# Performance work log

Measured on AMD Instinct MI355X. Metric: run time of the kernel, lower is better.

Reference implementation:

```python
import jax, jax.numpy as jnp
import numpy as np
import math

NUM_HEADS = 8
EMB = 256

def setup_inputs() -> dict:
    key = jax.random.key(0)
    ks = jax.random.split(key, 9)
    B_, N, C = 1024, 64, EMB  # 16 images * 64 windows, 8x8 window, C=256
    nW = 64
    q = jax.random.normal(ks[0], (B_, N, C), dtype=jnp.float32)
    k = jax.random.normal(ks[1], (B_, N, C), dtype=jnp.float32)
    v = jax.random.normal(ks[2], (B_, N, C), dtype=jnp.float32)
    mask = jax.random.normal(ks[3], (nW, N, N), dtype=jnp.float32)
    # MLP params (Linear: y = x @ W^T + b; we store W already transposed for x @ W)
    hid = 4 * C
    s1 = 1.0 / math.sqrt(C)
    s2 = 1.0 / math.sqrt(hid)
    w1 = jax.random.uniform(ks[4], (C, hid), minval=-s1, maxval=s1, dtype=jnp.float32)
    b1 = jax.random.uniform(ks[5], (hid,), minval=-s1, maxval=s1, dtype=jnp.float32)
    w2 = jax.random.uniform(ks[6], (hid, C), minval=-s2, maxval=s2, dtype=jnp.float32)
    b2 = jax.random.uniform(ks[7], (C,), minval=-s2, maxval=s2, dtype=jnp.float32)
    return {"q": q, "k": k, "v": v, "mask": mask, "H": 64, "W": 64,
            "w1": w1, "b1": b1, "w2": w2, "b2": b2}

def reference(q, k, v, mask, H, W, w1, b1, w2, b2):
    B_, N, C = q.shape
    h = NUM_HEADS
    d = C // h
    # separate heads: (B_, h, N, d)
    qh = q.reshape(B_, N, h, d).transpose(0, 2, 1, 3)
    kh = k.reshape(B_, N, h, d).transpose(0, 2, 1, 3)
    vh = v.reshape(B_, N, h, d).transpose(0, 2, 1, 3)
    attn = jnp.einsum('bhnd,bhmd->bhnm', qh, kh)  # raw scores
    nW = mask.shape[0]
    # additive window mask BEFORE scaling (faithful to original order)
    attn = attn.reshape(B_ // nW, nW, h, N, N) + mask[None, :, None, :, :]
    attn = attn.reshape(B_, h, N, N) / math.sqrt(d)
    attn = jax.nn.softmax(attn, axis=-1)
    out = jnp.einsum('bhnm,bhmd->bhnd', attn, vh)
    out = out.transpose(0, 2, 1, 3).reshape(B_, N, C)  # recombine heads
    # linear Mlp (dropout is identity at p=0.0); torch nn.GELU is exact erf
    hmid = jax.nn.gelu(out @ w1 + b1, approximate=False)
    out = out + (hmid @ w2 + b2)
    return out
```

## Files before the change

kernel.cpp:

```cpp
#include <hip/hip_runtime.h>
#include <hip/hip_bf16.h>
#include <cstdint>
#include <cstddef>

typedef __attribute__((ext_vector_type(8))) short bf16x8;
typedef __attribute__((ext_vector_type(4))) float f32x4;

static __device__ __forceinline__ unsigned short f2bf(float f) {
    __hip_bfloat16 h = __float2bfloat16(f);
    return *reinterpret_cast<unsigned short*>(&h);
}

static __device__ __forceinline__ f32x4 mfma_bf16(bf16x8 a, bf16x8 b, f32x4 c) {
    return __builtin_amdgcn_mfma_f32_16x16x32_bf16(a, b, c, 0, 0, 0);
}

static __device__ __forceinline__ bf16x8 pack8(float4 a, float4 b) {
    bf16x8 f;
    f[0]=(short)f2bf(a.x); f[1]=(short)f2bf(a.y); f[2]=(short)f2bf(a.z); f[3]=(short)f2bf(a.w);
    f[4]=(short)f2bf(b.x); f[5]=(short)f2bf(b.y); f[6]=(short)f2bf(b.z); f[7]=(short)f2bf(b.w);
    return f;
}

static __device__ __forceinline__ float gelu_erf(float v) {
    float s = v * 0.70710678118654752f;
    float a = fabsf(s);
    float t = __builtin_amdgcn_rcpf(1.0f + 0.3275911f * a);
    float poly = ((((1.061405429f * t - 1.453152027f) * t + 1.421413741f) * t
                   - 0.284496736f) * t + 0.254829592f) * t;
    float e = 1.0f - poly * __expf(-a * a);
    float erfv = copysignf(e, s);
    return 0.5f * v * (1.0f + erfv);
}

static __device__ __forceinline__ void load_lds16(const unsigned short* g, unsigned short* l) {
    __builtin_amdgcn_global_load_lds(
        (const __attribute__((address_space(1))) unsigned int*)g,
        (__attribute__((address_space(3))) unsigned int*)l, 16, 0, 0);
}

__global__ __launch_bounds__(256) void attn_kernel(
    const float* __restrict__ q, const float* __restrict__ k,
    const float* __restrict__ v, const float* __restrict__ mask,
    float* __restrict__ xout)
{
    __shared__ unsigned short Qs[64][40];
    __shared__ unsigned short Ks[64][40];
    __shared__ unsigned short Vt[32][72];
    __shared__ unsigned short Ps[64][72];

    const int tid  = threadIdx.x;
    const int b    = blockIdx.x >> 3;
    const int h    = blockIdx.x & 7;
    const int lane = tid & 63;
    const int l15  = lane & 15;
    const int g    = lane >> 4;
    const int w    = tid >> 6;

    {
        int row = tid >> 2;
        int seg = tid & 3;
        size_t base = ((size_t)(b * 64 + row)) * 256 + h * 32 + seg * 8;

        float4 a0 = *(const float4*)(q + base);
        float4 a1 = *(const float4*)(q + base + 4);
        unsigned short* p = &Qs[row][seg * 8];
        p[0]=f2bf(a0.x); p[1]=f2bf(a0.y); p[2]=f2bf(a0.z); p[3]=f2bf(a0.w);
        p[4]=f2bf(a1.x); p[5]=f2bf(a1.y); p[6]=f2bf(a1.z); p[7]=f2bf(a1.w);

        a0 = *(const float4*)(k + base);
        a1 = *(const float4*)(k + base + 4);
        p = &Ks[row][seg * 8];
        p[0]=f2bf(a0.x); p[1]=f2bf(a0.y); p[2]=f2bf(a0.z); p[3]=f2bf(a0.w);
        p[4]=f2bf(a1.x); p[5]=f2bf(a1.y); p[6]=f2bf(a1.z); p[7]=f2bf(a1.w);

        a0 = *(const float4*)(v + base);
        a1 = *(const float4*)(v + base + 4);
        int c = seg * 8;
        Vt[c + 0][row] = f2bf(a0.x);
        Vt[c + 1][row] = f2bf(a0.y);
        Vt[c + 2][row] = f2bf(a0.z);
        Vt[c + 3][row] = f2bf(a0.w);
        Vt[c + 4][row] = f2bf(a1.x);
        Vt[c + 5][row] = f2bf(a1.y);
        Vt[c + 6][row] = f2bf(a1.z);
        Vt[c + 7][row] = f2bf(a1.w);
    }
    __syncthreads();

    f32x4 s[4];
    {
        bf16x8 aQ = *(const bf16x8*)&Qs[w * 16 + l15][g * 8];
        #pragma unroll
        for (int ct = 0; ct < 4; ++ct) {
            bf16x8 bK = *(const bf16x8*)&Ks[ct * 16 + l15][g * 8];
            f32x4 z = {0.f, 0.f, 0.f, 0.f};
            s[ct] = mfma_bf16(aQ, bK, z);
        }
    }

    const float* mbase = mask + (size_t)(b & 63) * 4096;
    const float INV = 0.17677669529663688f;
    float rsum[4];
    #pragma unroll
    for (int r = 0; r < 4; ++r) {
        int row = w * 16 + g * 4 + r;
        float pr[4];
        #pragma unroll
        for (int ct = 0; ct < 4; ++ct)
            pr[ct] = (s[ct][r] + mbase[row * 64 + ct * 16 + l15]) * INV;
        float m = fmaxf(fmaxf(pr[0], pr[1]), fmaxf(pr[2], pr[3]));
        #pragma unroll
        for (int off = 1; off < 16; off <<= 1)
            m = fmaxf(m, __shfl_xor(m, off));
        float sum = 0.f;
        #pragma unroll
        for (int ct = 0; ct < 4; ++ct) { pr[ct] = __expf(pr[ct] - m); sum += pr[ct]; }
        #pragma unroll
        for (int off = 1; off < 16; off <<= 1)
            sum += __shfl_xor(sum, off);
        rsum[r] = sum;
        #pragma unroll
        for (int ct = 0; ct < 4; ++ct)
            Ps[row][ct * 16 + l15] = f2bf(pr[ct]);
    }

    f32x4 o[2] = {};
    #pragma unroll
    for (int ks = 0; ks < 2; ++ks) {
        bf16x8 pa = *(const bf16x8*)&Ps[w * 16 + l15][ks * 32 + g * 8];
        #pragma unroll
        for (int n = 0; n < 2; ++n) {
            bf16x8 vb = *(const bf16x8*)&Vt[n * 16 + l15][ks * 32 + g * 8];
            o[n] = mfma_bf16(pa, vb, o[n]);
        }
    }

    #pragma unroll
    for (int n = 0; n < 2; ++n) {
        #pragma unroll
        for (int r = 0; r < 4; ++r) {
            int row = w * 16 + g * 4 + r;
            xout[((size_t)(b * 64 + row)) * 256 + h * 32 + n * 16 + l15] =
                o[n][r] / rsum[r];
        }
    }
}

__global__ __launch_bounds__(256) void prep_w1(const float* __restrict__ src,
                                               unsigned short* __restrict__ dst)
{
    __shared__ float tile[64][65];
    const int kt = blockIdx.x, nb = blockIdx.y;
    const int t = threadIdx.x;
    const int r0 = t >> 4, c4 = (t & 15) * 4;
    #pragma unroll
    for (int p = 0; p < 4; ++p) {
        int kk = r0 + p * 16;
        float4 d = *(const float4*)(src + (size_t)(kt * 64 + kk) * 1024 + nb * 64 + c4);
        tile[kk][c4+0]=d.x; tile[kk][c4+1]=d.y; tile[kk][c4+2]=d.z; tile[kk][c4+3]=d.w;
    }
    __syncthreads();
    #pragma unroll
    for (int i = 0; i < 2; ++i) {
        int f = t + 256 * i;
        int chalf = f >> 8;
        int ksl   = (f >> 7) & 1;
        int nt    = (f >> 6) & 1;
        int gv    = (f >> 4) & 3;
        int l15v  = f & 15;
        int n_local = chalf * 32 + 8 * (l15v >> 2) + 4 * nt + (l15v & 3);
        int k_local = ksl * 32 + gv * 8;
        int c  = nb * 2 + chalf;
        int ks = kt * 2 + ksl;
        unsigned short tmp[8];
        #pragma unroll
        for (int e = 0; e < 8; ++e) tmp[e] = f2bf(tile[k_local + e][n_local]);
        size_t off = (size_t)c * 8192 + (size_t)((ks * 2 + nt) * 512)
                   + (gv * 16 + l15v) * 8;
        *(bf16x8*)(dst + off) = *(const bf16x8*)tmp;
    }
}

__global__ __launch_bounds__(256) void prep_w2(const float* __restrict__ src,
                                               unsigned short* __restrict__ dst)
{
    __shared__ float tile[64][65];
    const int ob = blockIdx.x, kb = blockIdx.y;
    const int t = threadIdx.x;
    const int r0 = t >> 4, c4 = (t & 15) * 4;
    #pragma unroll
    for (int p = 0; p < 4; ++p) {
        int kk = r0 + p * 16;
        float4 d = *(const float4*)(src + (size_t)(kb * 64 + kk) * 256 + ob * 64 + c4);
        tile[kk][c4+0]=d.x; tile[kk][c4+1]=d.y; tile[kk][c4+2]=d.z; tile[kk][c4+3]=d.w;
    }
    __syncthreads();
    #pragma unroll
    for (int i = 0; i < 2; ++i) {
        int f = t + 256 * i;
        int ksl = f >> 8;
        int tq  = (f >> 6) & 3;
        int gv  = (f >> 4) & 3;
        int l15v = f & 15;
        int c_local = tq * 16 + l15v;
        int k_local = ksl * 32 + gv * 8;
        int c = kb * 2 + ksl;
        unsigned short tmp[8];
        #pragma unroll
        for (int e = 0; e < 8; ++e) tmp[e] = f2bf(tile[k_local + e][c_local]);
        size_t off = (size_t)c * 8192 + (size_t)((ob * 4 + tq) * 512)
                   + (gv * 16 + l15v) * 8;
        *(bf16x8*)(dst + off) = *(const bf16x8*)tmp;
    }
}

__global__ __launch_bounds__(512, 4) void mlp_fused(
    const float* __restrict__ xin, float* __restrict__ xio,
    const unsigned short* __restrict__ wt1, const float* __restrict__ b1,
    const unsigned short* __restrict__ wt2, const float* __restrict__ b2)
{
    __shared__ unsigned short w1c[2][8192];
    __shared__ unsigned short w2c[2][8192];
    __shared__ float b1s[1024];

    const int tid  = threadIdx.x;
    const int lane = tid & 63;
    const int l15  = lane & 15;
    const int g    = lane >> 4;
    const int wid  = tid >> 6;
    const int fb   = (g * 16 + l15) * 8;

    const size_t rowbase = (size_t)blockIdx.x * 128;

    auto stage = [&](const unsigned short* gbase, unsigned short* lbase) {
        #pragma unroll
        for (int i = 0; i < 2; ++i) {
            load_lds16(gbase + (i * 512 + tid) * 8,
                       lbase + (i * 512 + wid * 64) * 8);
        }
    };

    stage(wt1, &w1c[0][0]);
    stage(wt2, &w2c[0][0]);

    b1s[tid]       = b1[tid];
    b1s[tid + 512] = b1[tid + 512];

    bf16x8 xf[8];
    {
        const float* xr = xin + (rowbase + wid * 16 + l15) * 256;
        #pragma unroll
        for (int ks = 0; ks < 8; ++ks) {
            float4 a0 = *(const float4*)(xr + ks * 32 + g * 8);
            float4 a1 = *(const float4*)(xr + ks * 32 + g * 8 + 4);
            xf[ks] = pack8(a0, a1);
        }
    }

    f32x4 oacc[16] = {};

    for (int hc = 0; hc < 32; ++hc) {
        const int cur = hc & 1;
        __syncthreads();

        if (hc < 31) {
            stage(wt1 + (size_t)(hc + 1) * 8192, &w1c[cur ^ 1][0]);
            stage(wt2 + (size_t)(hc + 1) * 8192, &w2c[cur ^ 1][0]);
        }

        f32x4 hacc[2] = {};
        #pragma unroll
        for (int ks = 0; ks < 8; ++ks) {
            bf16x8 w0 = *(const bf16x8*)&w1c[cur][(ks * 2 + 0) * 512 + fb];
            bf16x8 w1f = *(const bf16x8*)&w1c[cur][(ks * 2 + 1) * 512 + fb];
            hacc[0] = mfma_bf16(w0,  xf[ks], hacc[0]);
            hacc[1] = mfma_bf16(w1f, xf[ks], hacc[1]);
        }

        const float* bp = &b1s[hc * 32 + g * 8];
        float4 ba = *(const float4*)bp;
        float4 bb = *(const float4*)(bp + 4);
        bf16x8 aH;
        aH[0] = (short)f2bf(gelu_erf(hacc[0][0] + ba.x));
        aH[1] = (short)f2bf(gelu_erf(hacc[0][1] + ba.y));
        aH[2] = (short)f2bf(gelu_erf(hacc[0][2] + ba.z));
        aH[3] = (short)f2bf(gelu_erf(hacc[0][3] + ba.w));
        aH[4] = (short)f2bf(gelu_erf(hacc[1][0] + bb.x));
        aH[5] = (short)f2bf(gelu_erf(hacc[1][1] + bb.y));
        aH[6] = (short)f2bf(gelu_erf(hacc[1][2] + bb.z));
        aH[7] = (short)f2bf(gelu_erf(hacc[1][3] + bb.w));

        #pragma unroll
        for (int n = 0; n < 16; ++n) {
            bf16x8 bF = *(const bf16x8*)&w2c[cur][n * 512 + fb];
            oacc[n] = mfma_bf16(aH, bF, oacc[n]);
        }
    }

    #pragma unroll
    for (int n = 0; n < 16; ++n) {
        int col = n * 16 + l15;
        float bias = b2[col];
        #pragma unroll
        for (int r = 0; r < 4; ++r) {
            size_t idx = (rowbase + wid * 16 + g * 4 + r) * 256 + col;
            xio[idx] = oacc[n][r] + bias + xio[idx];
        }
    }
}

extern "C" void kernel_launch(void* const* d_in, const int* in_sizes, int n_in,
                              void* d_out, int out_size, void* d_ws, size_t ws_size,
                              hipStream_t stream)
{
    const float* q    = (const float*)d_in[0];
    const float* k    = (const float*)d_in[1];
    const float* v    = (const float*)d_in[2];
    const float* mask = (const float*)d_in[3];
    const float* w1   = (const float*)d_in[6];
    const float* b1   = (const float*)d_in[7];
    const float* w2   = (const float*)d_in[8];
    const float* b2   = (const float*)d_in[9];

    float* xio = (float*)d_out;

    unsigned short* wt1 = (unsigned short*)d_ws;
    unsigned short* wt2 = wt1 + (size_t)1024 * 256;

    prep_w1<<<dim3(4, 16), 256, 0, stream>>>(w1, wt1);
    prep_w2<<<dim3(4, 16), 256, 0, stream>>>(w2, wt2);

    attn_kernel<<<8192, 256, 0, stream>>>(q, k, v, mask, xio);

    mlp_fused<<<512, 512, 0, stream>>>(xio, xio, wt1, b1, wt2, b2);
}
```

Measured before the change: 170.0 us.

## Switch MLP kernel to 32x32x16 MFMA with 32-row wave tiles

The fused MLP kernel moves from 16x16x32 to 32x32x16 bf16 MFMA. Each wave now owns 32 rows and blocks shrink to 256 threads while still covering 128 rows. The weight-prep kernels are rewritten to emit the matching fragment layout, dropping the LDS transpose and using 32 blocks. The goal is fewer LDS fragment reads per FLOP and better MFMA efficiency, at the cost of more accumulator registers per wave (128 floats of output accumulators) and possibly lower occupancy.

```diff
diff --git a/kernel.cpp b/kernel.cpp
--- a/kernel.cpp
+++ b/kernel.cpp
@@ -5,6 +5,7 @@
 
 typedef __attribute__((ext_vector_type(8))) short bf16x8;
 typedef __attribute__((ext_vector_type(4))) float f32x4;
+typedef __attribute__((ext_vector_type(16))) float f32x16;
 
 static __device__ __forceinline__ unsigned short f2bf(float f) {
     __hip_bfloat16 h = __float2bfloat16(f);
@@ -13,6 +14,9 @@
 
 static __device__ __forceinline__ f32x4 mfma_bf16(bf16x8 a, bf16x8 b, f32x4 c) {
     return __builtin_amdgcn_mfma_f32_16x16x32_bf16(a, b, c, 0, 0, 0);
+}
+static __device__ __forceinline__ f32x16 mfma32(bf16x8 a, bf16x8 b, f32x16 c) {
+    return __builtin_amdgcn_mfma_f32_32x32x16_bf16(a, b, c, 0, 0, 0);
 }
 
 static __device__ __forceinline__ bf16x8 pack8(float4 a, float4 b) {
@@ -147,75 +151,52 @@
     }
 }
 
+static __device__ __forceinline__ int sigma32(int a) {
+    return ((a >> 4) & 1) * 16 + ((a >> 2) & 1) * 8 + ((a >> 3) & 1) * 4 + (a & 3);
+}
+
 __global__ __launch_bounds__(256) void prep_w1(const float* __restrict__ src,
                                                unsigned short* __restrict__ dst)
 {
-    __shared__ float tile[64][65];
-    const int kt = blockIdx.x, nb = blockIdx.y;
+    const int c = blockIdx.x;
     const int t = threadIdx.x;
-    const int r0 = t >> 4, c4 = (t & 15) * 4;
-    #pragma unroll
-    for (int p = 0; p < 4; ++p) {
-        int kk = r0 + p * 16;
-        float4 d = *(const float4*)(src + (size_t)(kt * 64 + kk) * 1024 + nb * 64 + c4);
-        tile[kk][c4+0]=d.x; tile[kk][c4+1]=d.y; tile[kk][c4+2]=d.z; tile[kk][c4+3]=d.w;
-    }
-    __syncthreads();
-    #pragma unroll
-    for (int i = 0; i < 2; ++i) {
-        int f = t + 256 * i;
-        int chalf = f >> 8;
-        int ksl   = (f >> 7) & 1;
-        int nt    = (f >> 6) & 1;
-        int gv    = (f >> 4) & 3;
-        int l15v  = f & 15;
-        int n_local = chalf * 32 + 8 * (l15v >> 2) + 4 * nt + (l15v & 3);
-        int k_local = ksl * 32 + gv * 8;
-        int c  = nb * 2 + chalf;
-        int ks = kt * 2 + ksl;
+    #pragma unroll
+    for (int i = 0; i < 4; ++i) {
+        int idx = i * 256 + t;
+        int ks  = idx >> 6;
+        int l   = idx & 63;
+        int l31 = l & 31, hi = l >> 5;
+        int n   = c * 32 + sigma32(l31);
         unsigned short tmp[8];
         #pragma unroll
-        for (int e = 0; e < 8; ++e) tmp[e] = f2bf(tile[k_local + e][n_local]);
-        size_t off = (size_t)c * 8192 + (size_t)((ks * 2 + nt) * 512)
-                   + (gv * 16 + l15v) * 8;
-        *(bf16x8*)(dst + off) = *(const bf16x8*)tmp;
+        for (int e = 0; e < 8; ++e)
+            tmp[e] = f2bf(src[(size_t)(ks * 16 + hi * 8 + e) * 1024 + n]);
+        *(bf16x8*)(dst + (size_t)c * 8192 + ks * 512 + l * 8) = *(const bf16x8*)tmp;
     }
 }
 
 __global__ __launch_bounds__(256) void prep_w2(const float* __restrict__ src,
                                                unsigned short* __restrict__ dst)
 {
-    __shared__ float tile[64][65];
-    const int ob = blockIdx.x, kb = blockIdx.y;
+    const int c = blockIdx.x;
     const int t = threadIdx.x;
-    const int r0 = t >> 4, c4 = (t & 15) * 4;
-    #pragma unroll
-    for (int p = 0; p < 4; ++p) {
-        int kk = r0 + p * 16;
-        float4 d = *(const float4*)(src + (size_t)(kb * 64 + kk) * 256 + ob * 64 + c4);
-        tile[kk][c4+0]=d.x; tile[kk][c4+1]=d.y; tile[kk][c4+2]=d.z; tile[kk][c4+3]=d.w;
-    }
-    __syncthreads();
-    #pragma unroll
-    for (int i = 0; i < 2; ++i) {
-        int f = t + 256 * i;
-        int ksl = f >> 8;
-        int tq  = (f >> 6) & 3;
-        int gv  = (f >> 4) & 3;
-        int l15v = f & 15;
-        int c_local = tq * 16 + l15v;
-        int k_local = ksl * 32 + gv * 8;
-        int c = kb * 2 + ksl;
+    #pragma unroll
+    for (int i = 0; i < 4; ++i) {
+        int idx  = i * 256 + t;
+        int span = idx >> 6;
+        int l    = idx & 63;
+        int n    = span >> 1;
+        int j    = span & 1;
+        int l31  = l & 31, hi = l >> 5;
         unsigned short tmp[8];
         #pragma unroll
-        for (int e = 0; e < 8; ++e) tmp[e] = f2bf(tile[k_local + e][c_local]);
-        size_t off = (size_t)c * 8192 + (size_t)((ob * 4 + tq) * 512)
-                   + (gv * 16 + l15v) * 8;
-        *(bf16x8*)(dst + off) = *(const bf16x8*)tmp;
-    }
-}
-
-__global__ __launch_bounds__(512, 4) void mlp_fused(
+        for (int e = 0; e < 8; ++e)
+            tmp[e] = f2bf(src[(size_t)(c * 32 + j * 16 + hi * 8 + e) * 256 + n * 32 + l31]);
+        *(bf16x8*)(dst + (size_t)c * 8192 + span * 512 + l * 8) = *(const bf16x8*)tmp;
+    }
+}
+
+__global__ __launch_bounds__(256, 2) void mlp_fused(
     const float* __restrict__ xin, float* __restrict__ xio,
     const unsigned short* __restrict__ wt1, const float* __restrict__ b1,
     const unsigned short* __restrict__ wt2, const float* __restrict__ b2)
@@ -226,18 +207,18 @@
 
     const int tid  = threadIdx.x;
     const int lane = tid & 63;
-    const int l15  = lane & 15;
-    const int g    = lane >> 4;
+    const int l31  = lane & 31;
+    const int hi   = lane >> 5;
     const int wid  = tid >> 6;
-    const int fb   = (g * 16 + l15) * 8;
-
-    const size_t rowbase = (size_t)blockIdx.x * 128;
+    const int fb   = lane * 8;
+
+    const size_t rowbase = (size_t)blockIdx.x * 128 + wid * 32;
 
     auto stage = [&](const unsigned short* gbase, unsigned short* lbase) {
         #pragma unroll
-        for (int i = 0; i < 2; ++i) {
-            load_lds16(gbase + (i * 512 + tid) * 8,
-                       lbase + (i * 512 + wid * 64) * 8);
+        for (int i = 0; i < 4; ++i) {
+            load_lds16(gbase + (i * 256 + tid) * 8,
+                       lbase + (i * 256 + wid * 64) * 8);
         }
     };
 
@@ -245,66 +226,79 @@
     stage(wt2, &w2c[0][0]);
 
     b1s[tid]       = b1[tid];
+    b1s[tid + 256] = b1[tid + 256];
     b1s[tid + 512] = b1[tid + 512];
-
-    bf16x8 xf[8];
+    b1s[tid + 768] = b1[tid + 768];
+
+    bf16x8 xf[16];
     {
-        const float* xr = xin + (rowbase + wid * 16 + l15) * 256;
-        #pragma unroll
-        for (int ks = 0; ks < 8; ++ks) {
-            float4 a0 = *(const float4*)(xr + ks * 32 + g * 8);
-            float4 a1 = *(const float4*)(xr + ks * 32 + g * 8 + 4);
+        const float* xr = xin + (rowbase + l31) * 256;
+        #pragma unroll
+        for (int ks = 0; ks < 16; ++ks) {
+            float4 a0 = *(const float4*)(xr + ks * 16 + hi * 8);
+            float4 a1 = *(const float4*)(xr + ks * 16 + hi * 8 + 4);
             xf[ks] = pack8(a0, a1);
         }
     }
 
-    f32x4 oacc[16] = {};
-
-    for (int hc = 0; hc < 32; ++hc) {
-        const int cur = hc & 1;
+    f32x16 oacc[8] = {};
+
+    for (int c = 0; c < 32; ++c) {
+        const int cur = c & 1;
         __syncthreads();
 
-        if (hc < 31) {
-            stage(wt1 + (size_t)(hc + 1) * 8192, &w1c[cur ^ 1][0]);
-            stage(wt2 + (size_t)(hc + 1) * 8192, &w2c[cur ^ 1][0]);
-        }
-
-        f32x4 hacc[2] = {};
-        #pragma unroll
-        for (int ks = 0; ks < 8; ++ks) {
-            bf16x8 w0 = *(const bf16x8*)&w1c[cur][(ks * 2 + 0) * 512 + fb];
-            bf16x8 w1f = *(const bf16x8*)&w1c[cur][(ks * 2 + 1) * 512 + fb];
-            hacc[0] = mfma_bf16(w0,  xf[ks], hacc[0]);
-            hacc[1] = mfma_bf16(w1f, xf[ks], hacc[1]);
-        }
-
-        const float* bp = &b1s[hc * 32 + g * 8];
-        float4 ba = *(const float4*)bp;
-        float4 bb = *(const float4*)(bp + 4);
-        bf16x8 aH;
-        aH[0] = (short)f2bf(gelu_erf(hacc[0][0] + ba.x));
-        aH[1] = (short)f2bf(gelu_erf(hacc[0][1] + ba.y));
-        aH[2] = (short)f2bf(gelu_erf(hacc[0][2] + ba.z));
-        aH[3] = (short)f2bf(gelu_erf(hacc[0][3] + ba.w));
-        aH[4] = (short)f2bf(gelu_erf(hacc[1][0] + bb.x));
-        aH[5] = (short)f2bf(gelu_erf(hacc[1][1] + bb.y));
-        aH[6] = (short)f2bf(gelu_erf(hacc[1][2] + bb.z));
-        aH[7] = (short)f2bf(gelu_erf(hacc[1][3] + bb.w));
-
-        #pragma unroll
-        for (int n = 0; n < 16; ++n) {
-            bf16x8 bF = *(const bf16x8*)&w2c[cur][n * 512 + fb];
-            oacc[n] = mfma_bf16(aH, bF, oacc[n]);
-        }
-    }
-
-    #pragma unroll
-    for (int n = 0; n < 16; ++n) {
-        int col = n * 16 + l15;
+        if (c < 31) {
+            stage(wt1 + (size_t)(c + 1) * 8192, &w1c[cur ^ 1][0]);
+            stage(wt2 + (size_t)(c + 1) * 8192, &w2c[cur ^ 1][0]);
+        }
+
+        f32x16 hacc = {};
+        #pragma unroll
+        for (int ks = 0; ks < 16; ++ks) {
+            bf16x8 wf = *(const bf16x8*)&w1c[cur][ks * 512 + fb];
+            hacc = mfma32(wf, xf[ks], hacc);
+        }
+
+        const float* bp = &b1s[c * 32 + hi * 8];
+        float4 ba0 = *(const float4*)(bp);
+        float4 ba1 = *(const float4*)(bp + 4);
+        float4 bb0 = *(const float4*)(bp + 16);
+        float4 bb1 = *(const float4*)(bp + 20);
+        bf16x8 aH0, aH1;
+        aH0[0] = (short)f2bf(gelu_erf(hacc[0]  + ba0.x));
+        aH0[1] = (short)f2bf(gelu_erf(hacc[1]  + ba0.y));
+        aH0[2] = (short)f2bf(gelu_erf(hacc[2]  + ba0.z));
+        aH0[3] = (short)f2bf(gelu_erf(hacc[3]  + ba0.w));
+        aH0[4] = (short)f2bf(gelu_erf(hacc[4]  + ba1.x));
+        aH0[5] = (short)f2bf(gelu_erf(hacc[5]  + ba1.y));
+        aH0[6] = (short)f2bf(gelu_erf(hacc[6]  + ba1.z));
+        aH0[7] = (short)f2bf(gelu_erf(hacc[7]  + ba1.w));
+        aH1[0] = (short)f2bf(gelu_erf(hacc[8]  + bb0.x));
+        aH1[1] = (short)f2bf(gelu_erf(hacc[9]  + bb0.y));
+        aH1[2] = (short)f2bf(gelu_erf(hacc[10] + bb0.z));
+        aH1[3] = (short)f2bf(gelu_erf(hacc[11] + bb0.w));
+        aH1[4] = (short)f2bf(gelu_erf(hacc[12] + bb1.x));
+        aH1[5] = (short)f2bf(gelu_erf(hacc[13] + bb1.y));
+        aH1[6] = (short)f2bf(gelu_erf(hacc[14] + bb1.z));
+        aH1[7] = (short)f2bf(gelu_erf(hacc[15] + bb1.w));
+
+        #pragma unroll
+        for (int n = 0; n < 8; ++n) {
+            bf16x8 bF0 = *(const bf16x8*)&w2c[cur][(n * 2 + 0) * 512 + fb];
+            bf16x8 bF1 = *(const bf16x8*)&w2c[cur][(n * 2 + 1) * 512 + fb];
+            oacc[n] = mfma32(aH0, bF0, oacc[n]);
+            oacc[n] = mfma32(aH1, bF1, oacc[n]);
+        }
+    }
+
+    #pragma unroll
+    for (int n = 0; n < 8; ++n) {
+        int col = n * 32 + l31;
         float bias = b2[col];
         #pragma unroll
-        for (int r = 0; r < 4; ++r) {
-            size_t idx = (rowbase + wid * 16 + g * 4 + r) * 256 + col;
+        for (int r = 0; r < 16; ++r) {
+            int row_local = (r & 3) + 8 * (r >> 2) + 4 * hi;
+            size_t idx = (rowbase + row_local) * 256 + col;
             xio[idx] = oacc[n][r] + bias + xio[idx];
         }
     }
@@ -328,10 +322,10 @@
     unsigned short* wt1 = (unsigned short*)d_ws;
     unsigned short* wt2 = wt1 + (size_t)1024 * 256;
 
-    prep_w1<<<dim3(4, 16), 256, 0, stream>>>(w1, wt1);
-    prep_w2<<<dim3(4, 16), 256, 0, stream>>>(w2, wt2);
+    prep_w1<<<32, 256, 0, stream>>>(w1, wt1);
+    prep_w2<<<32, 256, 0, stream>>>(w2, wt2);
 
     attn_kernel<<<8192, 256, 0, stream>>>(q, k, v, mask, xio);
 
-    mlp_fused<<<512, 512, 0, stream>>>(xio, xio, wt1, b1, wt2, b2);
-}
+    mlp_fused<<<512, 256, 0, stream>>>(xio, xio, wt1, b1, wt2, b2);
+}
```

Result: faster. 163.7 us (-3.7%).
